# Kernel optimization log

Hardware: AMD Instinct MI355X
Metric: run time of the kernel (lower is better)

The kernel has to match this reference:

```python
import jax, jax.numpy as jnp
import numpy as np


def _maxpool2(a):
    # MaxPool2d(kernel_size=2, stride=2) on NCHW
    return jax.lax.reduce_window(a, -jnp.inf, jax.lax.max,
                                 (1, 1, 2, 2), (1, 1, 2, 2), 'VALID')


def setup_inputs() -> dict:
    key = jax.random.key(0)
    k1, k2, k3, k4, k5 = jax.random.split(key, 5)
    B, C, H, W = 4, 128, 512, 512
    O = 64
    x = jax.random.normal(k1, (B, C, H, W), dtype=jnp.float32)
    # 1x1 conv weights stored as [out, in]; biases [out]
    Wk = jax.random.normal(k2, (O, C), dtype=jnp.float32) * 0.05
    bk = jax.random.normal(k3, (O,), dtype=jnp.float32) * 0.05
    Wv = jax.random.normal(k4, (O, C), dtype=jnp.float32) * 0.05
    bv = jax.random.normal(k5, (O,), dtype=jnp.float32) * 0.05
    return {"x": x, "Wk": Wk, "bk": bk, "Wv": Wv, "bv": bv}


def reference(x, Wk, bk, Wv, bv):
    # three 2x2 max pools -> downsample by 8
    p = _maxpool2(_maxpool2(_maxpool2(x)))            # [B, C, h, w], h=H/8
    # 1x1 convs
    k = jnp.einsum('bchw,oc->bohw', p, Wk) + bk[None, :, None, None]
    v = jnp.einsum('bchw,oc->bohw', p, Wv) + bv[None, :, None, None]
    # torch: attn = (value[n,:,None] @ key[n,None,:]).mean(axis over value idx)
    # attn[n, j] = mean_i v[n,i] * k[n,j] = mean(v[n]) * k[n,j]  (exact)
    vmean = v.mean(axis=(2, 3), keepdims=True)        # [B, O, 1, 1]
    attn = vmean * k                                   # [B, O, h, w]
    B, O, h, w = attn.shape
    # F.interpolate(..., mode='bilinear', align_corners=False) == jax bilinear resize
    out = jax.image.resize(attn, (B, O, h * 8, w * 8), method='bilinear')
    return out
```

## Files before the change

kernel.cpp:

```cpp
#include <hip/hip_runtime.h>
#include <math.h>

#define NB 4
#define NC 128
#define NO 64
#define HH 512
#define WW 512
#define PH 64
#define PW 64
#define PHW (PH*PW)

__global__ __launch_bounds__(256) void pool8(const float* __restrict__ x,
                                             float* __restrict__ p) {
    int idx = blockIdx.x * 256 + threadIdx.x;
    int w  = idx & (PW - 1);
    int h  = (idx >> 6) & (PH - 1);
    int bc = idx >> 12;
    const float* src = x + ((size_t)bc * HH + (size_t)h * 8) * WW + (size_t)w * 8;
    float m = -INFINITY;
#pragma unroll
    for (int r = 0; r < 8; ++r) {
        float4 a = *(const float4*)(src + (size_t)r * WW);
        float4 b = *(const float4*)(src + (size_t)r * WW + 4);
        m = fmaxf(m, fmaxf(fmaxf(a.x, a.y), fmaxf(a.z, a.w)));
        m = fmaxf(m, fmaxf(fmaxf(b.x, b.y), fmaxf(b.z, b.w)));
    }
    p[idx] = m;
}

__global__ __launch_bounds__(256) void psum_k(const float* __restrict__ p,
                                              float* __restrict__ psum) {
    int bc = blockIdx.x;
    const float* base = p + (size_t)bc * PHW;
    float s = 0.f;
    for (int i = threadIdx.x; i < PHW; i += 256) s += base[i];
#pragma unroll
    for (int off = 32; off > 0; off >>= 1) s += __shfl_down(s, off, 64);
    __shared__ float ls[4];
    int lane = threadIdx.x & 63, wid = threadIdx.x >> 6;
    if (lane == 0) ls[wid] = s;
    __syncthreads();
    if (threadIdx.x == 0) psum[bc] = ls[0] + ls[1] + ls[2] + ls[3];
}

__global__ void vmean_k(const float* __restrict__ psum, const float* __restrict__ Wv,
                        const float* __restrict__ bv, float* __restrict__ vmean) {
    int t = threadIdx.x;
    int b = t >> 6, o = t & 63;
    float s = 0.f;
    for (int c = 0; c < NC; ++c) s = fmaf(psum[b * NC + c], Wv[o * NC + c], s);
    vmean[t] = s * (1.f / (float)PHW) + bv[o];
}

__global__ __launch_bounds__(256) void attn_k(const float* __restrict__ p,
                                              const float* __restrict__ Wk,
                                              const float* __restrict__ bk,
                                              const float* __restrict__ vmean,
                                              float* __restrict__ attn) {
    int blk = blockIdx.x;
    int hwblk = blk & 15;
    int ot    = (blk >> 4) & 3;
    int b     = blk >> 6;
    int hw    = hwblk * 256 + threadIdx.x;
    int obase = ot * 16;
    const float* pb = p + (size_t)b * NC * PHW + hw;
    float acc[16];
#pragma unroll
    for (int o = 0; o < 16; ++o) acc[o] = 0.f;
    for (int c = 0; c < NC; ++c) {
        float val = pb[(size_t)c * PHW];
#pragma unroll
        for (int o = 0; o < 16; ++o)
            acc[o] = fmaf(val, Wk[(obase + o) * NC + c], acc[o]);
    }
#pragma unroll
    for (int o = 0; o < 16; ++o) {
        int oo = obase + o;
        attn[((size_t)(b * NO + oo)) * PHW + hw] =
            vmean[b * NO + oo] * (acc[o] + bk[oo]);
    }
}

__global__ __launch_bounds__(256) void upsample_k(const float* __restrict__ attn,
                                                  float* __restrict__ out) {
    int t  = blockIdx.x * 256 + threadIdx.x;
    int xq = t & 127;
    int y  = (t >> 7) & 511;
    int bo = t >> 16;
    float sy = (y + 0.5f) * 0.125f - 0.5f;
    float fy0 = floorf(sy);
    float fy = sy - fy0;
    int y0 = (int)fy0;
    int y1 = y0 + 1;
    y0 = max(y0, 0); y1 = min(y1, PH - 1);
    const float* row0 = attn + ((size_t)bo * PH + y0) * PW;
    const float* row1 = attn + ((size_t)bo * PH + y1) * PW;
    float4 res;
    float* rp = (float*)&res;
#pragma unroll
    for (int j = 0; j < 4; ++j) {
        int xx = xq * 4 + j;
        float sx = (xx + 0.5f) * 0.125f - 0.5f;
        float fx0 = floorf(sx);
        float fx = sx - fx0;
        int x0 = (int)fx0;
        int x1 = x0 + 1;
        x0 = max(x0, 0); x1 = min(x1, PW - 1);
        float a00 = row0[x0], a01 = row0[x1];
        float a10 = row1[x0], a11 = row1[x1];
        float top = a00 + fx * (a01 - a00);
        float bot = a10 + fx * (a11 - a10);
        rp[j] = top + fy * (bot - top);
    }
    *(float4*)(out + (size_t)t * 4) = res;
}

extern "C" void kernel_launch(void* const* d_in, const int* in_sizes, int n_in,
                              void* d_out, int out_size, void* d_ws, size_t ws_size,
                              hipStream_t stream) {
    const float* x  = (const float*)d_in[0];
    const float* Wk = (const float*)d_in[1];
    const float* bk = (const float*)d_in[2];
    const float* Wv = (const float*)d_in[3];
    const float* bv = (const float*)d_in[4];
    float* out = (float*)d_out;

    float* p     = (float*)d_ws;
    float* attn  = p + (size_t)NB * NC * PHW;
    float* psum  = attn + (size_t)NB * NO * PHW;
    float* vmean = psum + NB * NC;

    pool8<<<NB * NC * PHW / 256, 256, 0, stream>>>(x, p);
    psum_k<<<NB * NC, 256, 0, stream>>>(p, psum);
    vmean_k<<<1, 256, 0, stream>>>(psum, Wv, bv, vmean);
    attn_k<<<256, 256, 0, stream>>>(p, Wk, bk, vmean, attn);
    upsample_k<<<NB * NO * HH * WW / 4 / 256, 256, 0, stream>>>(attn, out);
}
```

Before: 810.6 us.

## Fuse channel sum into pooling, fold vmean into attn, restructure upsample

The pooling kernel now uses two threads per output, each reading one float4 per row, and combines them with a lane shuffle. It also reduces the block's pooled values and atomically adds them into per-channel sums, which removes the separate psum and vmean kernels. The vmean dot product moves into the attention kernel, where each block recomputes it for its own 16 output channels. The upsample kernel now produces 8 outputs per thread from a 2x3 neighbourhood, using fixed fractional weights instead of per-element floor math. In exchange it adds an atomic reduction with nondeterministic float summation order and an extra small zeroing launch.

```diff
diff --git a/kernel.cpp b/kernel.cpp
--- a/kernel.cpp
+++ b/kernel.cpp
@@ -10,52 +10,43 @@
 #define PW 64
 #define PHW (PH*PW)
 
+__global__ void zero_psum(float* __restrict__ psum) {
+    psum[threadIdx.x] = 0.f;
+}
+
 __global__ __launch_bounds__(256) void pool8(const float* __restrict__ x,
-                                             float* __restrict__ p) {
-    int idx = blockIdx.x * 256 + threadIdx.x;
-    int w  = idx & (PW - 1);
-    int h  = (idx >> 6) & (PH - 1);
-    int bc = idx >> 12;
-    const float* src = x + ((size_t)bc * HH + (size_t)h * 8) * WW + (size_t)w * 8;
+                                             float* __restrict__ p,
+                                             float* __restrict__ psum) {
+    int q  = blockIdx.x * 256 + threadIdx.x;
+    int wh = q & 127;
+    int h  = (q >> 7) & (PH - 1);
+    int bc = q >> 13;
+    const float* src = x + ((size_t)bc * HH + (size_t)h * 8) * WW + (size_t)wh * 4;
     float m = -INFINITY;
 #pragma unroll
     for (int r = 0; r < 8; ++r) {
         float4 a = *(const float4*)(src + (size_t)r * WW);
-        float4 b = *(const float4*)(src + (size_t)r * WW + 4);
         m = fmaxf(m, fmaxf(fmaxf(a.x, a.y), fmaxf(a.z, a.w)));
-        m = fmaxf(m, fmaxf(fmaxf(b.x, b.y), fmaxf(b.z, b.w)));
     }
-    p[idx] = m;
-}
+    float mm = fmaxf(m, __shfl_xor(m, 1, 64));
+    if (!(threadIdx.x & 1)) p[q >> 1] = mm;
 
-__global__ __launch_bounds__(256) void psum_k(const float* __restrict__ p,
-                                              float* __restrict__ psum) {
-    int bc = blockIdx.x;
-    const float* base = p + (size_t)bc * PHW;
-    float s = 0.f;
-    for (int i = threadIdx.x; i < PHW; i += 256) s += base[i];
+    float ps = (threadIdx.x & 1) ? 0.f : mm;
 #pragma unroll
-    for (int off = 32; off > 0; off >>= 1) s += __shfl_down(s, off, 64);
+    for (int off = 32; off > 0; off >>= 1) ps += __shfl_down(ps, off, 64);
     __shared__ float ls[4];
     int lane = threadIdx.x & 63, wid = threadIdx.x >> 6;
-    if (lane == 0) ls[wid] = s;
+    if (lane == 0) ls[wid] = ps;
     __syncthreads();
-    if (threadIdx.x == 0) psum[bc] = ls[0] + ls[1] + ls[2] + ls[3];
-}
-
-__global__ void vmean_k(const float* __restrict__ psum, const float* __restrict__ Wv,
-                        const float* __restrict__ bv, float* __restrict__ vmean) {
-    int t = threadIdx.x;
-    int b = t >> 6, o = t & 63;
-    float s = 0.f;
-    for (int c = 0; c < NC; ++c) s = fmaf(psum[b * NC + c], Wv[o * NC + c], s);
-    vmean[t] = s * (1.f / (float)PHW) + bv[o];
+    if (threadIdx.x == 0) atomicAdd(&psum[bc], ls[0] + ls[1] + ls[2] + ls[3]);
 }
 
 __global__ __launch_bounds__(256) void attn_k(const float* __restrict__ p,
                                               const float* __restrict__ Wk,
                                               const float* __restrict__ bk,
-                                              const float* __restrict__ vmean,
+                                              const float* __restrict__ Wv,
+                                              const float* __restrict__ bv,
+                                              const float* __restrict__ psum,
                                               float* __restrict__ attn) {
     int blk = blockIdx.x;
     int hwblk = blk & 15;
@@ -63,6 +54,17 @@
     int b     = blk >> 6;
     int hw    = hwblk * 256 + threadIdx.x;
     int obase = ot * 16;
+
+    __shared__ float vm[16];
+    if (threadIdx.x < 16) {
+        int oo = obase + threadIdx.x;
+        float s = 0.f;
+        for (int c = 0; c < NC; ++c)
+            s = fmaf(psum[b * NC + c], Wv[oo * NC + c], s);
+        vm[threadIdx.x] = s * (1.f / (float)PHW) + bv[oo];
+    }
+    __syncthreads();
+
     const float* pb = p + (size_t)b * NC * PHW + hw;
     float acc[16];
 #pragma unroll
@@ -76,43 +78,47 @@
 #pragma unroll
     for (int o = 0; o < 16; ++o) {
         int oo = obase + o;
-        attn[((size_t)(b * NO + oo)) * PHW + hw] =
-            vmean[b * NO + oo] * (acc[o] + bk[oo]);
+        attn[((size_t)(b * NO + oo)) * PHW + hw] = vm[o] * (acc[o] + bk[oo]);
     }
 }
 
 __global__ __launch_bounds__(256) void upsample_k(const float* __restrict__ attn,
                                                   float* __restrict__ out) {
     int t  = blockIdx.x * 256 + threadIdx.x;
-    int xq = t & 127;
-    int y  = (t >> 7) & 511;
-    int bo = t >> 16;
-    float sy = (y + 0.5f) * 0.125f - 0.5f;
-    float fy0 = floorf(sy);
-    float fy = sy - fy0;
-    int y0 = (int)fy0;
-    int y1 = y0 + 1;
-    y0 = max(y0, 0); y1 = min(y1, PH - 1);
-    const float* row0 = attn + ((size_t)bo * PH + y0) * PW;
-    const float* row1 = attn + ((size_t)bo * PH + y1) * PW;
-    float4 res;
-    float* rp = (float*)&res;
-#pragma unroll
-    for (int j = 0; j < 4; ++j) {
-        int xx = xq * 4 + j;
-        float sx = (xx + 0.5f) * 0.125f - 0.5f;
-        float fx0 = floorf(sx);
-        float fx = sx - fx0;
-        int x0 = (int)fx0;
-        int x1 = x0 + 1;
-        x0 = max(x0, 0); x1 = min(x1, PW - 1);
-        float a00 = row0[x0], a01 = row0[x1];
-        float a10 = row1[x0], a11 = row1[x1];
-        float top = a00 + fx * (a01 - a00);
-        float bot = a10 + fx * (a11 - a10);
-        rp[j] = top + fy * (bot - top);
-    }
-    *(float4*)(out + (size_t)t * 4) = res;
+    int k  = t & 63;
+    int y  = (t >> 6) & 511;
+    int bo = t >> 15;
+    int m  = y >> 3;
+    int i  = y & 7;
+    int ylo = (i < 4) ? m - 1 : m;
+    int r0 = max(ylo, 0);
+    int r1 = min(ylo + 1, PH - 1);
+    float fy = (float)((2 * i + 9) & 15) * 0.0625f;
+
+    const float* base = attn + (size_t)bo * PHW;
+    const float* row0 = base + r0 * PW;
+    const float* row1 = base + r1 * PW;
+    int xm1 = max(k - 1, 0);
+    int xp1 = min(k + 1, PW - 1);
+    float a0 = row0[xm1], a1 = row0[k], a2 = row0[xp1];
+    float b0 = row1[xm1], b1 = row1[k], b2 = row1[xp1];
+    float c0 = a0 + fy * (b0 - a0);
+    float c1 = a1 + fy * (b1 - a1);
+    float c2 = a2 + fy * (b2 - a2);
+    float d01 = c1 - c0;
+    float d12 = c2 - c1;
+    float4 lo, hi;
+    lo.x = c0 + (9.f  * 0.0625f) * d01;
+    lo.y = c0 + (11.f * 0.0625f) * d01;
+    lo.z = c0 + (13.f * 0.0625f) * d01;
+    lo.w = c0 + (15.f * 0.0625f) * d01;
+    hi.x = c1 + (1.f  * 0.0625f) * d12;
+    hi.y = c1 + (3.f  * 0.0625f) * d12;
+    hi.z = c1 + (5.f  * 0.0625f) * d12;
+    hi.w = c1 + (7.f  * 0.0625f) * d12;
+    float* dst = out + ((size_t)bo * HH + y) * WW + (size_t)k * 8;
+    *(float4*)dst = lo;
+    *(float4*)(dst + 4) = hi;
 }
 
 extern "C" void kernel_launch(void* const* d_in, const int* in_sizes, int n_in,
@@ -128,11 +134,9 @@
     float* p     = (float*)d_ws;
     float* attn  = p + (size_t)NB * NC * PHW;
     float* psum  = attn + (size_t)NB * NO * PHW;
-    float* vmean = psum + NB * NC;
 
-    pool8<<<NB * NC * PHW / 256, 256, 0, stream>>>(x, p);
-    psum_k<<<NB * NC, 256, 0, stream>>>(p, psum);
-    vmean_k<<<1, 256, 0, stream>>>(psum, Wv, bv, vmean);
-    attn_k<<<256, 256, 0, stream>>>(p, Wk, bk, vmean, attn);
-    upsample_k<<<NB * NO * HH * WW / 4 / 256, 256, 0, stream>>>(attn, out);
+    zero_psum<<<1, 512, 0, stream>>>(psum);
+    pool8<<<NB * NC * PHW * 2 / 256, 256, 0, stream>>>(x, p, psum);
+    attn_k<<<256, 256, 0, stream>>>(p, Wk, bk, Wv, bv, psum, attn);
+    upsample_k<<<NB * NO * HH * PW / 256, 256, 0, stream>>>(attn, out);
 }
```

After: 814.3 us. Within noise of the previous version (+0.5%).
